# Kernel optimization log

Measured on AMD Instinct MI355X. Metric: run time of the kernel, lower is better.

Reference implementation:

```python
import jax, jax.numpy as jnp
import numpy as np

N = 50000   # nodes
E = 800000  # edges
F = 64      # input features
H = 64      # hidden (nhid)
C = 10      # classes
G = 500     # graphs in batch


def setup_inputs() -> dict:
    key = jax.random.key(0)
    ks = jax.random.split(key, 12)
    s = lambda fan: np.float32(1.0 / np.sqrt(fan))
    return {
        "x": jax.random.normal(ks[0], (N, F), jnp.float32),
        "edge_index": jax.random.randint(ks[1], (2, E), 0, N, dtype=jnp.int64),
        "batch": jnp.sort(jax.random.randint(ks[2], (N,), 0, G, dtype=jnp.int64)),
        "W1": jax.random.normal(ks[3], (F, H), jnp.float32) * s(F),
        "b1": jnp.zeros((H,), jnp.float32),
        "W2": jax.random.normal(ks[4], (H, H), jnp.float32) * s(H),
        "b2": jnp.zeros((H,), jnp.float32),
        "W3": jax.random.normal(ks[5], (H, H), jnp.float32) * s(H),
        "b3": jnp.zeros((H,), jnp.float32),
        "lin1_W": jax.random.normal(ks[6], (H, H), jnp.float32) * s(H),
        "lin1_b": jnp.zeros((H,), jnp.float32),
        "lin2_W": jax.random.normal(ks[7], (H, C), jnp.float32) * s(H),
        "lin2_b": jnp.zeros((C,), jnp.float32),
    }


def reference(x, edge_index, batch, W1, b1, W2, b2, W3, b3, lin1_W, lin1_b, lin2_W, lin2_b):
    n = x.shape[0]
    loops = jnp.arange(n, dtype=edge_index.dtype)
    src = jnp.concatenate([edge_index[0], loops])  # message sources (x_j)
    dst = jnp.concatenate([edge_index[1], loops])  # aggregation targets
    # symmetric GCN normalization on A + I
    deg = jax.ops.segment_sum(jnp.ones(src.shape, x.dtype), dst, num_segments=n)
    dis = jax.lax.rsqrt(deg)  # deg >= 1 thanks to self-loops
    norm = (dis[src] * dis[dst])[:, None]  # [E+N, 1]

    def gcn_relu(h, W, b):
        h = h @ W                                   # [N, H]
        agg = jax.ops.segment_sum(h[src] * norm, dst, num_segments=n)
        return jax.nn.relu(agg + b)

    h = gcn_relu(x, W1, b1)
    h = gcn_relu(h, W2, b2)
    h = gcn_relu(h, W3, b3)

    # global mean pool per graph
    sums = jax.ops.segment_sum(h, batch, num_segments=G)
    counts = jax.ops.segment_sum(jnp.ones((n,), h.dtype), batch, num_segments=G)
    pooled = sums / jnp.maximum(counts, 1.0)[:, None]  # [G, H]

    h = jax.nn.relu(pooled @ lin1_W + lin1_b)
    # dropout is identity in eval mode
    logits = h @ lin2_W + lin2_b
    return jax.nn.log_softmax(logits, axis=-1)
```

## Files before the change

kernel.cpp:

```cpp
#include <hip/hip_runtime.h>

#define NN 50000
#define NE 800000
#define HD 64
#define NC 10
#define NG 500
#define CAP 64
#define CAPR 32
#define NBLK 196
#define NPART 8
#define PSZ 6250
#define FILLB 2048
#define MBLK 782

typedef float f32x4 __attribute__((ext_vector_type(4)));
typedef short bf16x8 __attribute__((ext_vector_type(8)));

__device__ __forceinline__ float bf16_to_f32(unsigned short h) {
    union { unsigned int u; float f; } v;
    v.u = ((unsigned int)h) << 16;
    return v.f;
}
__device__ __forceinline__ unsigned short f32_to_bf16(float f) {
    union { float f; unsigned int u; } v;
    v.f = f;
    unsigned int r = v.u + 0x7FFFu + ((v.u >> 16) & 1u);
    return (unsigned short)(r >> 16);
}

__device__ __forceinline__ float gather_relu(
    const unsigned short* __restrict__ tin, const unsigned short* __restrict__ ovf,
    int wid, int colv, int sel, int c0, float di, float bv, int lane) {
    int cnt = c0 > CAP ? CAP : c0;
    int cmain = cnt > CAPR ? CAPR : cnt;
    float acc[8];
#pragma unroll
    for (int j = 0; j < 8; ++j) acc[j] = 0.f;
    acc[0] = bf16_to_f32(tin[(size_t)wid * HD + lane]);
    int e = 0;
    for (; e + 7 < cmain; e += 8) {
#pragma unroll
        for (int j = 0; j < 8; ++j) {
            int s = __shfl(colv, sel + e + j);
            acc[j] += bf16_to_f32(tin[(size_t)s * HD + lane]);
        }
    }
    for (; e < cmain; ++e) {
        int s = __shfl(colv, sel + e);
        acc[0] += bf16_to_f32(tin[(size_t)s * HD + lane]);
    }
    if (cnt > CAPR) {
        int co = ovf[(size_t)wid * CAPR + (lane & 31)];
        for (int e2 = CAPR; e2 < cnt; ++e2) {
            int s = __shfl(co, e2 - CAPR);
            acc[0] += bf16_to_f32(tin[(size_t)s * HD + lane]);
        }
    }
    float s01 = (acc[0] + acc[1]) + (acc[2] + acc[3]);
    float s23 = (acc[4] + acc[5]) + (acc[6] + acc[7]);
    return fmaxf((s01 + s23) * di + bv, 0.f);
}

__device__ __forceinline__ void load_wfrags(const float* __restrict__ W, int lane,
                                            bf16x8 bh[4][2], bf16x8 bl[4][2]) {
    int col = lane & 15, krow = (lane >> 4) * 8;
#pragma unroll
    for (int n = 0; n < 4; ++n)
#pragma unroll
        for (int kt = 0; kt < 2; ++kt)
#pragma unroll
            for (int j = 0; j < 8; ++j) {
                float wv = W[(kt * 32 + krow + j) * 64 + n * 16 + col];
                unsigned short h = f32_to_bf16(wv);
                float rem = wv - bf16_to_f32(h);
                bh[n][kt][j] = (short)h;
                bl[n][kt][j] = (short)f32_to_bf16(rem);
            }
}

__global__ void init_k(int* __restrict__ rowcnt, float* __restrict__ pooled) {
    int i = blockIdx.x * 256 + threadIdx.x;
    if (i < NN) rowcnt[i] = 0;
    if (i < NG * HD) pooled[i] = 0.f;
}

__global__ __launch_bounds__(256) void fill3_k(
    const int* __restrict__ src, const int* __restrict__ dst,
    int* __restrict__ rowcnt, unsigned short* __restrict__ col32,
    unsigned short* __restrict__ ovf) {
    int part = blockIdx.x & (NPART - 1);
    int blk = blockIdx.x >> 3;
    int dlo = part * PSZ, dhi = dlo + PSZ;
    int stride = (FILLB / NPART) * 256;
    for (int e = blk * 256 + threadIdx.x; e < NE; e += stride) {
        int d = dst[e];
        if (d >= dlo && d < dhi) {
            int p = atomicAdd(&rowcnt[d], 1);
            if (p < CAPR) col32[(size_t)d * CAPR + p] = (unsigned short)src[e];
            else if (p < CAP) ovf[(size_t)d * CAPR + (p - CAPR)] = (unsigned short)src[e];
        }
    }
}

__global__ __launch_bounds__(256) void mfma_gemm1_k(
    const float* __restrict__ x, const float* __restrict__ W,
    const int* __restrict__ rowcnt, unsigned short* __restrict__ out16) {
    __shared__ unsigned short A[64][72];
    int t = threadIdx.x, lane = t & 63, w = t >> 6;
    int base = blockIdx.x * 64;
#pragma unroll
    for (int i = 0; i < 4; ++i) {
        int idx = t + i * 256;
        int row = idx >> 4, c4 = (idx & 15) * 4;
        int r = base + row;
        float4 v = make_float4(0.f, 0.f, 0.f, 0.f);
        if (r < NN) v = ((const float4*)x)[(size_t)r * 16 + (idx & 15)];
        unsigned int p0 = f32_to_bf16(v.x) | ((unsigned int)f32_to_bf16(v.y) << 16);
        unsigned int p1 = f32_to_bf16(v.z) | ((unsigned int)f32_to_bf16(v.w) << 16);
        *(unsigned int*)&A[row][c4] = p0;
        *(unsigned int*)&A[row][c4 + 2] = p1;
    }
    bf16x8 bh[4][2], bl[4][2];
    load_wfrags(W, lane, bh, bl);
    __syncthreads();
    int col = lane & 15, krow = (lane >> 4) * 8;
    bf16x8 a0 = *(const bf16x8*)&A[w * 16 + col][krow];
    bf16x8 a1 = *(const bf16x8*)&A[w * 16 + col][32 + krow];
    f32x4 acc[4];
#pragma unroll
    for (int n = 0; n < 4; ++n) { acc[n] = (f32x4){0.f, 0.f, 0.f, 0.f}; }
#pragma unroll
    for (int n = 0; n < 4; ++n) {
        acc[n] = __builtin_amdgcn_mfma_f32_16x16x32_bf16(a0, bh[n][0], acc[n], 0, 0, 0);
        acc[n] = __builtin_amdgcn_mfma_f32_16x16x32_bf16(a1, bh[n][1], acc[n], 0, 0, 0);
        acc[n] = __builtin_amdgcn_mfma_f32_16x16x32_bf16(a0, bl[n][0], acc[n], 0, 0, 0);
        acc[n] = __builtin_amdgcn_mfma_f32_16x16x32_bf16(a1, bl[n][1], acc[n], 0, 0, 0);
    }
    int row0 = base + w * 16 + (lane >> 4) * 4;
    float di[4];
#pragma unroll
    for (int r = 0; r < 4; ++r)
        di[r] = (row0 + r < NN) ? rsqrtf((float)(rowcnt[row0 + r] + 1)) : 1.f;
#pragma unroll
    for (int n = 0; n < 4; ++n)
#pragma unroll
        for (int r = 0; r < 4; ++r) {
            int row = row0 + r;
            if (row < NN)
                out16[(size_t)row * HD + n * 16 + col] = f32_to_bf16(acc[n][r] * di[r]);
        }
}

__global__ __launch_bounds__(512) void agg_mfma_k(
    const unsigned short* __restrict__ tin, const int* __restrict__ rowcnt,
    const unsigned short* __restrict__ col32, const unsigned short* __restrict__ ovf,
    const float* __restrict__ bias, const float* __restrict__ W,
    unsigned short* __restrict__ tout) {
    __shared__ unsigned short A[64][72];
    __shared__ unsigned short Whi[64][72];
    __shared__ unsigned short Wlo[64][72];
    __shared__ float dibuf[64];
    int t = threadIdx.x, lane = t & 63, w = t >> 6;
    int base = blockIdx.x * 64;
    float bv = bias[lane];
    int cidx = base + w * 8 + (lane & 7);
    int cnt8 = rowcnt[cidx < NN ? cidx : NN - 1];
    int colv2[4];
#pragma unroll
    for (int np = 0; np < 4; ++np) {
        int wid2 = base + w * 8 + np * 2 + (lane >= 32 ? 1 : 0);
        if (wid2 >= NN) wid2 = NN - 1;
        colv2[np] = col32[(size_t)wid2 * CAPR + (lane & 31)];
    }
    int c0[8];
#pragma unroll
    for (int n = 0; n < 8; ++n) {
        int v = __shfl(cnt8, n);
        c0[n] = (base + w * 8 + n < NN) ? v : -1;
    }
#pragma unroll
    for (int i = 0; i < 8; ++i) {
        int idx = t + i * 512;
        int k = idx >> 6, c = idx & 63;
        float wv = W[idx];
        unsigned short h = f32_to_bf16(wv);
        Whi[c][k] = h;
        Wlo[c][k] = f32_to_bf16(wv - bf16_to_f32(h));
    }
#pragma unroll
    for (int n = 0; n < 8; ++n) {
        int row = w * 8 + n;
        float r = 0.f, di = 1.f;
        if (c0[n] >= 0) {
            di = rsqrtf((float)(c0[n] + 1));
            r = gather_relu(tin, ovf, base + row, colv2[n >> 1], (n & 1) * 32,
                            c0[n], di, bv, lane);
        }
        A[row][lane] = f32_to_bf16(r);
        if (lane == 0) dibuf[row] = di;
    }
    __syncthreads();
    if (w >= 4) return;
    int col = lane & 15, krow = (lane >> 4) * 8;
    bf16x8 a0 = *(const bf16x8*)&A[w * 16 + col][krow];
    bf16x8 a1 = *(const bf16x8*)&A[w * 16 + col][32 + krow];
    float dr[4];
#pragma unroll
    for (int r = 0; r < 4; ++r) dr[r] = dibuf[w * 16 + (lane >> 4) * 4 + r];
    int row0 = base + w * 16 + (lane >> 4) * 4;
#pragma unroll
    for (int n = 0; n < 4; ++n) {
        bf16x8 bh0 = *(const bf16x8*)&Whi[n * 16 + col][krow];
        bf16x8 bh1 = *(const bf16x8*)&Whi[n * 16 + col][32 + krow];
        bf16x8 bl0 = *(const bf16x8*)&Wlo[n * 16 + col][krow];
        bf16x8 bl1 = *(const bf16x8*)&Wlo[n * 16 + col][32 + krow];
        f32x4 acc = (f32x4){0.f, 0.f, 0.f, 0.f};
        acc = __builtin_amdgcn_mfma_f32_16x16x32_bf16(a0, bh0, acc, 0, 0, 0);
        acc = __builtin_amdgcn_mfma_f32_16x16x32_bf16(a1, bh1, acc, 0, 0, 0);
        acc = __builtin_amdgcn_mfma_f32_16x16x32_bf16(a0, bl0, acc, 0, 0, 0);
        acc = __builtin_amdgcn_mfma_f32_16x16x32_bf16(a1, bl1, acc, 0, 0, 0);
#pragma unroll
        for (int r = 0; r < 4; ++r) {
            int row = row0 + r;
            if (row < NN)
                tout[(size_t)row * HD + n * 16 + col] = f32_to_bf16(acc[r] * dr[r]);
        }
    }
}

__global__ __launch_bounds__(512) void agg_pool_k(
    const unsigned short* __restrict__ tin, const int* __restrict__ rowcnt,
    const unsigned short* __restrict__ col32, const unsigned short* __restrict__ ovf,
    const float* __restrict__ bias, const int* __restrict__ batch,
    float* __restrict__ pooled) {
    int t = threadIdx.x, lane = t & 63, w = t >> 6;
    int base = blockIdx.x * 64 + w * 8;
    float bv = bias[lane];
    int cidx = base + (lane & 7);
    int cnt8 = rowcnt[cidx < NN ? cidx : NN - 1];
    int colv2[4];
#pragma unroll
    for (int np = 0; np < 4; ++np) {
        int wid2 = base + np * 2 + (lane >= 32 ? 1 : 0);
        if (wid2 >= NN) wid2 = NN - 1;
        colv2[np] = col32[(size_t)wid2 * CAPR + (lane & 31)];
    }
    int c0[8];
#pragma unroll
    for (int n = 0; n < 8; ++n) {
        int v = __shfl(cnt8, n);
        c0[n] = (base + n < NN) ? v : -1;
    }
    int curg = -1;
    float psum = 0.f;
#pragma unroll
    for (int n = 0; n < 8; ++n) {
        if (c0[n] >= 0) {
            int wid = base + n;
            float di = rsqrtf((float)(c0[n] + 1));
            float r = gather_relu(tin, ovf, wid, colv2[n >> 1], (n & 1) * 32,
                                  c0[n], di, bv, lane);
            int g = batch[wid];
            if (g != curg) {
                if (curg >= 0) atomicAdd(&pooled[(size_t)curg * HD + lane], psum);
                curg = g;
                psum = r;
            } else {
                psum += r;
            }
        }
    }
    if (curg >= 0) atomicAdd(&pooled[(size_t)curg * HD + lane], psum);
}

__global__ __launch_bounds__(64) void poolhead_k(
    const float* __restrict__ pooled, const int* __restrict__ batch,
    const float* __restrict__ l1W, const float* __restrict__ l1b,
    const float* __restrict__ l2W, const float* __restrict__ l2b,
    float* __restrict__ out) {
    __shared__ float p[64];
    __shared__ float hsm[64];
    __shared__ float lg[NC];
    __shared__ int ss[2];
    int g = blockIdx.x, t = threadIdx.x;
    if (t < 2) {
        int target = g + t;
        int lo = 0, hi = NN;
        while (lo < hi) {
            int mid = (lo + hi) >> 1;
            if (batch[mid] < target) lo = mid + 1; else hi = mid;
        }
        ss[t] = lo;
    }
    __syncthreads();
    float c = (float)(ss[1] - ss[0]);
    p[t] = pooled[(size_t)g * HD + t] / fmaxf(c, 1.0f);
    __syncthreads();
    float a = l1b[t];
#pragma unroll
    for (int k = 0; k < 64; ++k) a += p[k] * l1W[k * 64 + t];
    hsm[t] = fmaxf(a, 0.f);
    __syncthreads();
    if (t < NC) {
        float a2 = l2b[t];
#pragma unroll
        for (int k = 0; k < 64; ++k) a2 += hsm[k] * l2W[k * NC + t];
        lg[t] = a2;
    }
    __syncthreads();
    if (t < NC) {
        float m = -1e30f;
#pragma unroll
        for (int k = 0; k < NC; ++k) m = fmaxf(m, lg[k]);
        float s = 0.f;
#pragma unroll
        for (int k = 0; k < NC; ++k) s += expf(lg[k] - m);
        out[(size_t)g * NC + t] = lg[t] - m - logf(s);
    }
}

extern "C" void kernel_launch(void* const* d_in, const int* in_sizes, int n_in,
                              void* d_out, int out_size, void* d_ws, size_t ws_size,
                              hipStream_t stream) {
    const float* x = (const float*)d_in[0];
    const int* ei = (const int*)d_in[1];
    const int* src = ei;
    const int* dst = ei + NE;
    const int* batch = (const int*)d_in[2];
    const float* W1 = (const float*)d_in[3];
    const float* b1 = (const float*)d_in[4];
    const float* W2 = (const float*)d_in[5];
    const float* b2 = (const float*)d_in[6];
    const float* W3 = (const float*)d_in[7];
    const float* b3 = (const float*)d_in[8];
    const float* l1W = (const float*)d_in[9];
    const float* l1b = (const float*)d_in[10];
    const float* l2W = (const float*)d_in[11];
    const float* l2b = (const float*)d_in[12];
    float* out = (float*)d_out;

    char* p = (char*)d_ws;
    auto alloc = [&](size_t bytes) {
        char* r = p;
        p += (bytes + 255) & ~(size_t)255;
        return r;
    };
    int* rowcnt = (int*)alloc(NN * 4);
    unsigned short* col32 = (unsigned short*)alloc((size_t)NN * CAPR * 2);
    unsigned short* ovf = (unsigned short*)alloc((size_t)NN * CAPR * 2);
    unsigned short* tmpA = (unsigned short*)alloc((size_t)NN * HD * 2);
    unsigned short* tmpB = (unsigned short*)alloc((size_t)NN * HD * 2);
    float* pooled = (float*)alloc((size_t)NG * HD * 4);

    init_k<<<NBLK, 256, 0, stream>>>(rowcnt, pooled);
    fill3_k<<<FILLB, 256, 0, stream>>>(src, dst, rowcnt, col32, ovf);

    mfma_gemm1_k<<<MBLK, 256, 0, stream>>>(x, W1, rowcnt, tmpA);
    agg_mfma_k<<<MBLK, 512, 0, stream>>>(tmpA, rowcnt, col32, ovf, b1, W2, tmpB);
    agg_mfma_k<<<MBLK, 512, 0, stream>>>(tmpB, rowcnt, col32, ovf, b2, W3, tmpA);
    agg_pool_k<<<MBLK, 512, 0, stream>>>(tmpA, rowcnt, col32, ovf, b3, batch, pooled);

    poolhead_k<<<NG, 64, 0, stream>>>(pooled, batch, l1W, l1b, l2W, l2b, out);
}
```

Before: 229.8 us.

## Split bf16 feature tables into two 32-column planes and gather two rows per wave

Stores the intermediate node feature tables as two 32-column half-planes instead of one 64-wide row-major array. Each wave now gathers neighbours for two nodes at once, one per 32-lane half, and walks the two planes in sequence. The aim is a smaller per-pass gather working set (about 3.2 MB per plane) that fits cache better, and denser 64-byte row accesses. In exchange, each half-wave loops to the larger of the two neighbour counts with masked loads, which wastes some lanes when degrees differ.

```diff
diff --git a/kernel.cpp b/kernel.cpp
--- a/kernel.cpp
+++ b/kernel.cpp
@@ -12,6 +12,7 @@
 #define PSZ 6250
 #define FILLB 2048
 #define MBLK 782
+#define PLANE ((size_t)NN * 32)
 
 typedef float f32x4 __attribute__((ext_vector_type(4)));
 typedef short bf16x8 __attribute__((ext_vector_type(8)));
@@ -28,37 +29,50 @@
     return (unsigned short)(r >> 16);
 }
 
-__device__ __forceinline__ float gather_relu(
-    const unsigned short* __restrict__ tin, const unsigned short* __restrict__ ovf,
-    int wid, int colv, int sel, int c0, float di, float bv, int lane) {
-    int cnt = c0 > CAP ? CAP : c0;
-    int cmain = cnt > CAPR ? CAPR : cnt;
+__device__ __forceinline__ float pair_gather(
+    const unsigned short* __restrict__ tp, const unsigned short* __restrict__ ovf,
+    int widA, int colv, int cA, int cB, int lane) {
+    int mine = (lane >> 5) & 1;
+    int wid = widA + mine;
+    int cm = mine ? cB : cA;
+    int widc = (cm >= 0) ? wid : 0;
+    int c = lane & 31;
+    int cmn = cm < 0 ? 0 : (cm > CAPR ? CAPR : cm);
+    int cmax = cA > cB ? cA : cB;
+    if (cmax > CAPR) cmax = CAPR;
+    if (cmax < 0) cmax = 0;
     float acc[8];
 #pragma unroll
     for (int j = 0; j < 8; ++j) acc[j] = 0.f;
-    acc[0] = bf16_to_f32(tin[(size_t)wid * HD + lane]);
+    if (cm >= 0) acc[0] = bf16_to_f32(tp[(size_t)widc * 32 + c]);
     int e = 0;
-    for (; e + 7 < cmain; e += 8) {
+    for (; e + 7 < cmax; e += 8) {
 #pragma unroll
         for (int j = 0; j < 8; ++j) {
-            int s = __shfl(colv, sel + e + j);
-            acc[j] += bf16_to_f32(tin[(size_t)s * HD + lane]);
-        }
-    }
-    for (; e < cmain; ++e) {
-        int s = __shfl(colv, sel + e);
-        acc[0] += bf16_to_f32(tin[(size_t)s * HD + lane]);
-    }
-    if (cnt > CAPR) {
-        int co = ovf[(size_t)wid * CAPR + (lane & 31)];
-        for (int e2 = CAPR; e2 < cnt; ++e2) {
-            int s = __shfl(co, e2 - CAPR);
-            acc[0] += bf16_to_f32(tin[(size_t)s * HD + lane]);
+            int s = __shfl(colv, (lane & 32) + e + j);
+            float v = bf16_to_f32(tp[(size_t)s * 32 + c]);
+            acc[j] += (e + j < cmn) ? v : 0.f;
+        }
+    }
+    for (; e < cmax; ++e) {
+        int s = __shfl(colv, (lane & 32) + e);
+        float v = bf16_to_f32(tp[(size_t)s * 32 + c]);
+        acc[0] += (e < cmn) ? v : 0.f;
+    }
+    if (cA > CAPR || cB > CAPR) {
+        int co = ovf[(size_t)widc * CAPR + c];
+        int cfull = cm > CAP ? CAP : cm;
+        int tmax = (cA > cB ? cA : cB);
+        if (tmax > CAP) tmax = CAP;
+        for (int e2 = CAPR; e2 < tmax; ++e2) {
+            int s = __shfl(co, (lane & 32) + e2 - CAPR);
+            float v = bf16_to_f32(tp[(size_t)s * 32 + c]);
+            acc[0] += (e2 < cfull) ? v : 0.f;
         }
     }
     float s01 = (acc[0] + acc[1]) + (acc[2] + acc[3]);
     float s23 = (acc[4] + acc[5]) + (acc[6] + acc[7]);
-    return fmaxf((s01 + s23) * di + bv, 0.f);
+    return s01 + s23;
 }
 
 __device__ __forceinline__ void load_wfrags(const float* __restrict__ W, int lane,
@@ -147,7 +161,8 @@
         for (int r = 0; r < 4; ++r) {
             int row = row0 + r;
             if (row < NN)
-                out16[(size_t)row * HD + n * 16 + col] = f32_to_bf16(acc[n][r] * di[r]);
+                out16[(size_t)(n >> 1) * PLANE + (size_t)row * 32 + (n & 1) * 16 + col] =
+                    f32_to_bf16(acc[n][r] * di[r]);
         }
 }
 
@@ -162,7 +177,7 @@
     __shared__ float dibuf[64];
     int t = threadIdx.x, lane = t & 63, w = t >> 6;
     int base = blockIdx.x * 64;
-    float bv = bias[lane];
+    float bvh[2] = {bias[lane & 31], bias[32 + (lane & 31)]};
     int cidx = base + w * 8 + (lane & 7);
     int cnt8 = rowcnt[cidx < NN ? cidx : NN - 1];
     int colv2[4];
@@ -187,17 +202,22 @@
         Whi[c][k] = h;
         Wlo[c][k] = f32_to_bf16(wv - bf16_to_f32(h));
     }
-#pragma unroll
-    for (int n = 0; n < 8; ++n) {
-        int row = w * 8 + n;
-        float r = 0.f, di = 1.f;
-        if (c0[n] >= 0) {
-            di = rsqrtf((float)(c0[n] + 1));
-            r = gather_relu(tin, ovf, base + row, colv2[n >> 1], (n & 1) * 32,
-                            c0[n], di, bv, lane);
-        }
-        A[row][lane] = f32_to_bf16(r);
-        if (lane == 0) dibuf[row] = di;
+    int mine = (lane >> 5) & 1;
+#pragma unroll
+    for (int h = 0; h < 2; ++h) {
+        const unsigned short* tp = tin + (size_t)h * PLANE;
+#pragma unroll
+        for (int np = 0; np < 4; ++np) {
+            int widA = base + w * 8 + 2 * np;
+            float raw = pair_gather(tp, ovf, widA, colv2[np],
+                                    c0[2 * np], c0[2 * np + 1], lane);
+            int cm = mine ? c0[2 * np + 1] : c0[2 * np];
+            float di = rsqrtf((float)((cm < 0 ? 0 : cm) + 1));
+            float r = cm >= 0 ? fmaxf(raw * di + bvh[h], 0.f) : 0.f;
+            A[w * 8 + 2 * np + mine][h * 32 + (lane & 31)] = f32_to_bf16(r);
+            if (h == 0 && (lane & 31) == 0)
+                dibuf[w * 8 + 2 * np + mine] = cm >= 0 ? di : 1.f;
+        }
     }
     __syncthreads();
     if (w >= 4) return;
@@ -223,7 +243,8 @@
         for (int r = 0; r < 4; ++r) {
             int row = row0 + r;
             if (row < NN)
-                tout[(size_t)row * HD + n * 16 + col] = f32_to_bf16(acc[r] * dr[r]);
+                tout[(size_t)(n >> 1) * PLANE + (size_t)row * 32 + (n & 1) * 16 + col] =
+                    f32_to_bf16(acc[r] * dr[r]);
         }
     }
 }
@@ -235,7 +256,7 @@
     float* __restrict__ pooled) {
     int t = threadIdx.x, lane = t & 63, w = t >> 6;
     int base = blockIdx.x * 64 + w * 8;
-    float bv = bias[lane];
+    float bvh[2] = {bias[lane & 31], bias[32 + (lane & 31)]};
     int cidx = base + (lane & 7);
     int cnt8 = rowcnt[cidx < NN ? cidx : NN - 1];
     int colv2[4];
@@ -251,26 +272,34 @@
         int v = __shfl(cnt8, n);
         c0[n] = (base + n < NN) ? v : -1;
     }
-    int curg = -1;
-    float psum = 0.f;
-#pragma unroll
-    for (int n = 0; n < 8; ++n) {
-        if (c0[n] >= 0) {
-            int wid = base + n;
-            float di = rsqrtf((float)(c0[n] + 1));
-            float r = gather_relu(tin, ovf, wid, colv2[n >> 1], (n & 1) * 32,
-                                  c0[n], di, bv, lane);
-            int g = batch[wid];
+    int mine = (lane >> 5) & 1;
+#pragma unroll
+    for (int h = 0; h < 2; ++h) {
+        const unsigned short* tp = tin + (size_t)h * PLANE;
+        int curg = -1;
+        float psum = 0.f;
+#pragma unroll
+        for (int np = 0; np < 4; ++np) {
+            int widA = base + 2 * np;
+            float raw = pair_gather(tp, ovf, widA, colv2[np],
+                                    c0[2 * np], c0[2 * np + 1], lane);
+            int cm = mine ? c0[2 * np + 1] : c0[2 * np];
+            float di = rsqrtf((float)((cm < 0 ? 0 : cm) + 1));
+            float r = cm >= 0 ? fmaxf(raw * di + bvh[h], 0.f) : 0.f;
+            int wid = widA + mine;
+            int g = cm >= 0 ? batch[wid] : curg;
             if (g != curg) {
-                if (curg >= 0) atomicAdd(&pooled[(size_t)curg * HD + lane], psum);
+                if (curg >= 0)
+                    atomicAdd(&pooled[(size_t)curg * HD + h * 32 + (lane & 31)], psum);
                 curg = g;
                 psum = r;
             } else {
                 psum += r;
             }
         }
-    }
-    if (curg >= 0) atomicAdd(&pooled[(size_t)curg * HD + lane], psum);
+        if (curg >= 0)
+            atomicAdd(&pooled[(size_t)curg * HD + h * 32 + (lane & 31)], psum);
+    }
 }
 
 __global__ __launch_bounds__(64) void poolhead_k(
@@ -348,8 +377,8 @@
     int* rowcnt = (int*)alloc(NN * 4);
     unsigned short* col32 = (unsigned short*)alloc((size_t)NN * CAPR * 2);
     unsigned short* ovf = (unsigned short*)alloc((size_t)NN * CAPR * 2);
-    unsigned short* tmpA = (unsigned short*)alloc((size_t)NN * HD * 2);
-    unsigned short* tmpB = (unsigned short*)alloc((size_t)NN * HD * 2);
+    unsigned short* tmpA = (unsigned short*)alloc(2 * PLANE * 2);
+    unsigned short* tmpB = (unsigned short*)alloc(2 * PLANE * 2);
     float* pooled = (float*)alloc((size_t)NG * HD * 4);
 
     init_k<<<NBLK, 256, 0, stream>>>(rowcnt, pooled);
```

Measured after the change: 303.6 us. 32.1% more time.

## Bucket edges by destination partition before CSR fill to avoid 8x edge rescans

Applied to the files above, without the earlier changes.

Replaces the fill kernel, in which each of 8 partition groups rescanned all edges, with two passes. A bucketing kernel first packs (dst,src) pairs into per-partition buffers using shared-memory counts and global atomics. A second kernel then fills the per-row neighbour lists, reading only its own partition's edges. This removes the redundant reads of the full src/dst arrays but adds a kernel launch, an intermediate buffer write and read, and a fixed per-partition capacity (ECAP) that could truncate edges under skewed input.

```diff
diff --git a/kernel.cpp b/kernel.cpp
--- a/kernel.cpp
+++ b/kernel.cpp
@@ -10,8 +10,10 @@
 #define NBLK 196
 #define NPART 8
 #define PSZ 6250
-#define FILLB 2048
 #define MBLK 782
+#define EBLK 1024
+#define EPER 782
+#define ECAP 102400
 
 typedef float f32x4 __attribute__((ext_vector_type(4)));
 typedef short bf16x8 __attribute__((ext_vector_type(8)));
@@ -78,27 +80,71 @@
             }
 }
 
-__global__ void init_k(int* __restrict__ rowcnt, float* __restrict__ pooled) {
+__global__ void init_k(int* __restrict__ rowcnt, float* __restrict__ pooled,
+                       int* __restrict__ pcnt) {
     int i = blockIdx.x * 256 + threadIdx.x;
     if (i < NN) rowcnt[i] = 0;
     if (i < NG * HD) pooled[i] = 0.f;
-}
-
-__global__ __launch_bounds__(256) void fill3_k(
+    if (i < NPART) pcnt[i] = 0;
+}
+
+__global__ __launch_bounds__(256) void bucket_k(
     const int* __restrict__ src, const int* __restrict__ dst,
+    int* __restrict__ pcnt, unsigned int* __restrict__ ebuf) {
+    __shared__ int lcnt[NPART];
+    __shared__ int lbase[NPART];
+    __shared__ int loff[NPART];
+    int t = threadIdx.x;
+    if (t < NPART) lcnt[t] = 0;
+    __syncthreads();
+    int e0 = blockIdx.x * EPER;
+    int e1 = e0 + EPER;
+    if (e1 > NE) e1 = NE;
+    int dd[4], sd[4], pd[4];
+    bool vv[4];
+#pragma unroll
+    for (int i = 0; i < 4; ++i) {
+        int e = e0 + t + i * 256;
+        bool v = e < e1;
+        vv[i] = v;
+        dd[i] = v ? dst[e] : 0;
+        sd[i] = v ? src[e] : 0;
+        pd[i] = dd[i] / PSZ;
+        if (v) atomicAdd(&lcnt[pd[i]], 1);
+    }
+    __syncthreads();
+    if (t < NPART) {
+        lbase[t] = atomicAdd(&pcnt[t], lcnt[t]);
+        loff[t] = 0;
+    }
+    __syncthreads();
+#pragma unroll
+    for (int i = 0; i < 4; ++i) {
+        if (vv[i]) {
+            int p = pd[i];
+            int pos = lbase[p] + atomicAdd(&loff[p], 1);
+            if (pos < ECAP)
+                ebuf[(size_t)p * ECAP + pos] =
+                    ((unsigned int)dd[i] << 16) | (unsigned int)sd[i];
+        }
+    }
+}
+
+__global__ __launch_bounds__(256) void fillp_k(
+    const unsigned int* __restrict__ ebuf, const int* __restrict__ pcnt,
     int* __restrict__ rowcnt, unsigned short* __restrict__ col32,
     unsigned short* __restrict__ ovf) {
     int part = blockIdx.x & (NPART - 1);
     int blk = blockIdx.x >> 3;
-    int dlo = part * PSZ, dhi = dlo + PSZ;
-    int stride = (FILLB / NPART) * 256;
-    for (int e = blk * 256 + threadIdx.x; e < NE; e += stride) {
-        int d = dst[e];
-        if (d >= dlo && d < dhi) {
-            int p = atomicAdd(&rowcnt[d], 1);
-            if (p < CAPR) col32[(size_t)d * CAPR + p] = (unsigned short)src[e];
-            else if (p < CAP) ovf[(size_t)d * CAPR + (p - CAPR)] = (unsigned short)src[e];
-        }
+    int n = pcnt[part];
+    if (n > ECAP) n = ECAP;
+    const unsigned int* eb = ebuf + (size_t)part * ECAP;
+    for (int i = blk * 256 + threadIdx.x; i < n; i += 256 * 256) {
+        unsigned int v = eb[i];
+        int d = v >> 16, s = v & 0xffff;
+        int p = atomicAdd(&rowcnt[d], 1);
+        if (p < CAPR) col32[(size_t)d * CAPR + p] = (unsigned short)s;
+        else if (p < CAP) ovf[(size_t)d * CAPR + (p - CAPR)] = (unsigned short)s;
     }
 }
 
@@ -351,9 +397,12 @@
     unsigned short* tmpA = (unsigned short*)alloc((size_t)NN * HD * 2);
     unsigned short* tmpB = (unsigned short*)alloc((size_t)NN * HD * 2);
     float* pooled = (float*)alloc((size_t)NG * HD * 4);
-
-    init_k<<<NBLK, 256, 0, stream>>>(rowcnt, pooled);
-    fill3_k<<<FILLB, 256, 0, stream>>>(src, dst, rowcnt, col32, ovf);
+    int* pcnt = (int*)alloc(NPART * 4);
+    unsigned int* ebuf = (unsigned int*)alloc((size_t)NPART * ECAP * 4);
+
+    init_k<<<NBLK, 256, 0, stream>>>(rowcnt, pooled, pcnt);
+    bucket_k<<<EBLK, 256, 0, stream>>>(src, dst, pcnt, ebuf);
+    fillp_k<<<2048, 256, 0, stream>>>(ebuf, pcnt, rowcnt, col32, ovf);
 
     mfma_gemm1_k<<<MBLK, 256, 0, stream>>>(x, W1, rowcnt, tmpA);
     agg_mfma_k<<<MBLK, 512, 0, stream>>>(tmpA, rowcnt, col32, ovf, b1, W2, tmpB);
```

New measurement: 240.4 us. +4.6%, slower.
